# Performance work log

Hardware: AMD Instinct MI355X
Metric: run time of the kernel (lower is better)

The kernel has to match this reference:

```python
import jax, jax.numpy as jnp
import numpy as np

N_HEADS = 4
HEAD_DIM = 6
D_MODEL = 24


def setup_inputs() -> dict:
    key = jax.random.key(0)
    ks = jax.random.split(key, 7)
    B, Tq, Tk = 16, 1024, 1024
    X = jax.random.normal(ks[0], (B, Tq, D_MODEL), dtype=jnp.float32)
    X_en = jax.random.normal(ks[1], (B, Tk, D_MODEL), dtype=jnp.float32)
    I_m = jax.random.randint(ks[2], (B, Tq, Tk), 0, 2, dtype=jnp.int32)
    scale = 1.0 / np.sqrt(D_MODEL)
    Wq = jax.random.normal(ks[3], (D_MODEL, D_MODEL), dtype=jnp.float32) * scale
    Wk = jax.random.normal(ks[4], (D_MODEL, D_MODEL), dtype=jnp.float32) * scale
    Wv = jax.random.normal(ks[5], (D_MODEL, D_MODEL), dtype=jnp.float32) * scale
    Wo = jax.random.normal(ks[6], (D_MODEL, D_MODEL), dtype=jnp.float32) * scale
    return {"X": X, "X_en": X_en, "I_m": I_m, "Wq": Wq, "Wk": Wk, "Wv": Wv, "Wo": Wo}


def _split_heads(x):
    # [B, T, 24] -> [B, 4, T, 6]
    B, T, _ = x.shape
    return x.reshape(B, T, N_HEADS, HEAD_DIM).transpose(0, 2, 1, 3)


def reference(X, X_en, I_m, Wq, Wk, Wv, Wo):
    # torch Linear (no bias): x @ W.T
    Q = _split_heads(X @ Wq.T)      # [B, H, Tq, d]
    K = _split_heads(X_en @ Wk.T)   # [B, H, Tk, d]
    V = _split_heads(X_en @ Wv.T)   # [B, H, Tk, d]
    scale = 1.0 / jnp.sqrt(jnp.asarray(HEAD_DIM, dtype=Q.dtype))
    A = jnp.einsum('bhqd,bhkd->bhqk', Q, K) * scale
    # NOTE: the original torch code calls A.masked_fill(...) without assigning
    # the result, so the mask I_m has NO effect. Faithfully reproduced here.
    A = jax.nn.softmax(A, axis=-1)
    O = jnp.einsum('bhqk,bhkd->bhqd', A, V)  # [B, H, Tq, d]
    B, H, Tq, d = O.shape
    O = O.transpose(0, 2, 1, 3).reshape(B, Tq, H * d)  # [B, Tq, 24]
    return O @ Wo.T
```

## Files before the change

### kernel.cpp

```cpp
#include <hip/hip_runtime.h>
#include <hip/hip_bf16.h>

#define NB 16
#define TT 1024
#define NH 4
#define HD 6
#define DM 24

#define QSC 0.5889785f
#define MBIAS 32.0f

typedef float v2f __attribute__((ext_vector_type(2)));
typedef short bf16x8 __attribute__((ext_vector_type(8)));
typedef float f32x16 __attribute__((ext_vector_type(16)));
typedef unsigned u32x2 __attribute__((ext_vector_type(2)));

__device__ __forceinline__ unsigned cvt_pk_bf16(float lo, float hi) {
  unsigned r;
  asm("v_cvt_pk_bf16_f32 %0, %1, %2" : "=v"(r) : "v"(lo), "v"(hi));
  return r;
}

__device__ __forceinline__ bf16x8 as_bf16x8(uint4 u) {
  union { uint4 u; bf16x8 b; } c;
  c.u = u;
  return c.b;
}

__device__ __forceinline__ unsigned short bf16of(float v) {
  union { __hip_bfloat16 b; unsigned short u; } c;
  c.b = __float2bfloat16(v);
  return c.u;
}

__device__ __forceinline__ float dot24(const float4* r,
                                       const float* __restrict__ w) {
  v2f a = {0.f, 0.f};
#pragma unroll
  for (int i = 0; i < 6; ++i) {
    v2f xp, wp;
    xp.x = r[i].x; xp.y = r[i].y;
    wp.x = w[4 * i + 0]; wp.y = w[4 * i + 1];
    a = __builtin_elementwise_fma(xp, wp, a);
    xp.x = r[i].z; xp.y = r[i].w;
    wp.x = w[4 * i + 2]; wp.y = w[4 * i + 3];
    a = __builtin_elementwise_fma(xp, wp, a);
  }
  return a.x + a.y;
}

__global__ __launch_bounds__(256, 4) void kvproj_kernel(
    const float* __restrict__ Xen, const float* __restrict__ Wk,
    const float* __restrict__ Wv, uint4* __restrict__ Kg,
    unsigned short* __restrict__ Vt) {
  const int gid = blockIdx.x * 256 + threadIdx.x;
  const int bh = gid >> 10;
  const int key = gid & (TT - 1);
  const int b = bh >> 2, h = bh & 3;
  const float* __restrict__ wkh = Wk + h * HD * DM;
  const float* __restrict__ wvh = Wv + h * HD * DM;
  const float4* __restrict__ xa =
      (const float4*)(Xen + ((size_t)b * TT + key) * DM);
  float4 xr[6];
#pragma unroll
  for (int i = 0; i < 6; ++i) xr[i] = xa[i];
  float kk[HD], vv[HD];
#pragma unroll
  for (int d = 0; d < HD; ++d) {
    kk[d] = dot24(xr, wkh + d * DM);
    vv[d] = dot24(xr, wvh + d * DM);
  }
  uint4* __restrict__ kdst = Kg + ((size_t)bh * TT + key) * 2;
  kdst[0] = make_uint4(cvt_pk_bf16(kk[0], kk[1]), cvt_pk_bf16(kk[2], kk[3]),
                       cvt_pk_bf16(kk[4], kk[5]), 0u);
  kdst[1] = make_uint4(0u, 0u, 0u, 0u);
  unsigned short* __restrict__ vrow = Vt + (size_t)bh * (7 * TT);
#pragma unroll
  for (int d = 0; d < HD; ++d) vrow[d * TT + key] = bf16of(vv[d]);
  vrow[6 * TT + key] = 0x3F80u;
}

__global__ __launch_bounds__(256, 4) void attn_mfma32_kernel(
    const float* __restrict__ X, const float* __restrict__ Wq,
    const uint4* __restrict__ Kg, const unsigned short* __restrict__ Vt,
    float* __restrict__ P) {
  const int ks = blockIdx.x & 1;
  const int tile = (blockIdx.x >> 1) & 7;
  const int bh = blockIdx.x >> 4;
  const int b = bh >> 2, h = bh & 3;
  const int lane = threadIdx.x & 63;
  const int w = threadIdx.x >> 6;
  const int hi = lane >> 5;
  const int qc = lane & 31;
  const int q = tile * 128 + w * 32 + qc;

  const float* __restrict__ wqh = Wq + h * HD * DM;
  uint4 uq = make_uint4(0u, 0u, 0u, 0u);
  if (hi == 0) {
    const float4* __restrict__ xq =
        (const float4*)(X + ((size_t)b * TT + q) * DM);
    float4 xr[6];
#pragma unroll
    for (int i = 0; i < 6; ++i) xr[i] = xq[i];
    float qv[HD];
#pragma unroll
    for (int d = 0; d < HD; ++d) qv[d] = dot24(xr, wqh + d * DM) * QSC;
    uq = make_uint4(cvt_pk_bf16(qv[0], qv[1]), cvt_pk_bf16(qv[2], qv[3]),
                    cvt_pk_bf16(qv[4], qv[5]), 0u);
  }
  const bf16x8 qfrag = as_bf16x8(uq);

  f32x16 cmb, oacc;
#pragma unroll
  for (int i = 0; i < 16; ++i) { cmb[i] = -MBIAS; oacc[i] = 0.f; }

  const uint4* __restrict__ kp =
      Kg + (size_t)bh * (TT * 2) + (size_t)ks * TT + qc * 2 + hi;
  const int dcl = (qc < 7) ? qc : 6;
  const uint4* __restrict__ vp =
      (const uint4*)(Vt + (size_t)bh * (7 * TT) + dcl * TT) + ks * 64 + hi;

#pragma unroll 2
  for (int it = 0; it < 16; ++it) {
    const uint4 ka = kp[it * 64];
    const uint4 va = vp[it * 4];
    const uint4 vb = vp[it * 4 + 2];

    f32x16 s = __builtin_amdgcn_mfma_f32_32x32x16_bf16(as_bf16x8(ka), qfrag,
                                                       cmb, 0, 0, 0);
    float p[16];
#pragma unroll
    for (int i = 0; i < 16; ++i) p[i] = __builtin_amdgcn_exp2f(s[i]);
    const unsigned c01 = cvt_pk_bf16(p[0], p[1]);
    const unsigned c23 = cvt_pk_bf16(p[2], p[3]);
    const unsigned c45 = cvt_pk_bf16(p[4], p[5]);
    const unsigned c67 = cvt_pk_bf16(p[6], p[7]);
    const unsigned c89 = cvt_pk_bf16(p[8], p[9]);
    const unsigned cAB = cvt_pk_bf16(p[10], p[11]);
    const unsigned cCD = cvt_pk_bf16(p[12], p[13]);
    const unsigned cEF = cvt_pk_bf16(p[14], p[15]);
    const u32x2 r0 = __builtin_amdgcn_permlane32_swap(c01, c45, false, false);
    const u32x2 r1 = __builtin_amdgcn_permlane32_swap(c23, c67, false, false);
    const u32x2 r2 = __builtin_amdgcn_permlane32_swap(c89, cCD, false, false);
    const u32x2 r3 = __builtin_amdgcn_permlane32_swap(cAB, cEF, false, false);
    const uint4 pb0 = make_uint4(r0[0], r1[0], r0[1], r1[1]);
    const uint4 pb1 = make_uint4(r2[0], r3[0], r2[1], r3[1]);
    oacc = __builtin_amdgcn_mfma_f32_32x32x16_bf16(as_bf16x8(va),
                                                   as_bf16x8(pb0), oacc, 0, 0, 0);
    oacc = __builtin_amdgcn_mfma_f32_32x32x16_bf16(as_bf16x8(vb),
                                                   as_bf16x8(pb1), oacc, 0, 0, 0);
  }

  const float a4 = __shfl_xor(oacc[0], 32);
  const float a5 = __shfl_xor(oacc[1], 32);
  const float ll = __shfl_xor(oacc[2], 32);
  if (hi == 0) {
    float* __restrict__ Pr =
        P + (((size_t)(bh * 2 + ks)) * TT + q) * 8;
    ((float4*)Pr)[0] = make_float4(ll, oacc[0], oacc[1], oacc[2]);
    ((float4*)Pr)[1] = make_float4(oacc[3], a4, a5, 0.f);
  }
}

__global__ __launch_bounds__(256, 4) void combine_outproj_kernel(
    const float* __restrict__ P, const float* __restrict__ Wo,
    float* __restrict__ out) {
  __shared__ float wsh[DM * DM];
  __shared__ float o[32][25];
  for (int i = threadIdx.x; i < DM * DM; i += 256) wsh[i] = Wo[i];
  const int r0 = blockIdx.x * 32;
  {
    const int unit = threadIdx.x >> 1, e = threadIdx.x & 1;
    const int rl = unit >> 2, h = unit & 3;
    const int r = r0 + rl, b = r >> 10, t = r & (TT - 1);
    const int bh = b * NH + h;
    const float4* __restrict__ pp =
        (const float4*)(P + (((size_t)(bh * 2 + e)) * TT + t) * 8);
    float4 x0 = pp[0], x1 = pp[1];
    float l = x0.x, a0 = x0.y, a1 = x0.z, a2 = x0.w;
    float a3 = x1.x, a4 = x1.y, a5 = x1.z;
    l += __shfl_xor(l, 1);
    a0 += __shfl_xor(a0, 1);
    a1 += __shfl_xor(a1, 1);
    a2 += __shfl_xor(a2, 1);
    a3 += __shfl_xor(a3, 1);
    a4 += __shfl_xor(a4, 1);
    a5 += __shfl_xor(a5, 1);
    if (e == 0) {
      const float inv = 1.f / l;
      o[rl][h * HD + 0] = a0 * inv;
      o[rl][h * HD + 1] = a1 * inv;
      o[rl][h * HD + 2] = a2 * inv;
      o[rl][h * HD + 3] = a3 * inv;
      o[rl][h * HD + 4] = a4 * inv;
      o[rl][h * HD + 5] = a5 * inv;
    }
  }
  __syncthreads();
  const int rl = threadIdx.x >> 3, u = threadIdx.x & 7;
  const int r = r0 + rl;
  float x[DM];
#pragma unroll
  for (int c = 0; c < DM; ++c) x[c] = o[rl][c];
#pragma unroll
  for (int jj = 0; jj < 3; ++jj) {
    const int j = u * 3 + jj;
    float a = 0.f;
#pragma unroll
    for (int c = 0; c < DM; ++c) a = fmaf(x[c], wsh[j * DM + c], a);
    out[(size_t)r * DM + j] = a;
  }
}

extern "C" void kernel_launch(void* const* d_in, const int* in_sizes, int n_in,
                              void* d_out, int out_size, void* d_ws, size_t ws_size,
                              hipStream_t stream) {
  const float* X = (const float*)d_in[0];
  const float* Xen = (const float*)d_in[1];
  const float* Wq = (const float*)d_in[3];
  const float* Wk = (const float*)d_in[4];
  const float* Wv = (const float*)d_in[5];
  const float* Wo = (const float*)d_in[6];

  char* ws = (char*)d_ws;
  float* P = (float*)ws;
  uint4* Kg = (uint4*)(ws + 4u * 1024 * 1024);
  unsigned short* Vt =
      (unsigned short*)(ws + 6u * 1024 * 1024);

  kvproj_kernel<<<NB * NH * TT / 256, 256, 0, stream>>>(Xen, Wk, Wv, Kg, Vt);
  attn_mfma32_kernel<<<NB * NH * 8 * 2, 256, 0, stream>>>(X, Wq, Kg, Vt, P);
  combine_outproj_kernel<<<NB * TT / 32, 256, 0, stream>>>(P, Wo,
                                                           (float*)d_out);
}
```

Measured before the change: 28.85 us.

## Switch attention to 16x16x32 MFMA tiles with compact K layout

Replaces the 32x32x16 bf16 MFMA attention kernel with one built on 16x16x32 MFMAs. Each wave now handles 16 queries, the grid doubles, and the launch bound rises to 8 blocks per SM. The K buffer drops its zero-padded second uint4 per key, which halves K traffic, and P fragments are rearranged with permlane32/permlane16 swaps. Partial-output layout and workspace offsets change to match. This cuts wasted MFMA work on the padded 32-wide dimension and raises occupancy, but the Q projection is now computed redundantly by more lanes.

```diff
diff --git a/kernel.cpp b/kernel.cpp
--- a/kernel.cpp
+++ b/kernel.cpp
@@ -12,7 +12,7 @@
 
 typedef float v2f __attribute__((ext_vector_type(2)));
 typedef short bf16x8 __attribute__((ext_vector_type(8)));
-typedef float f32x16 __attribute__((ext_vector_type(16)));
+typedef float f32x4 __attribute__((ext_vector_type(4)));
 typedef unsigned u32x2 __attribute__((ext_vector_type(2)));
 
 __device__ __forceinline__ unsigned cvt_pk_bf16(float lo, float hi) {
@@ -70,33 +70,36 @@
     kk[d] = dot24(xr, wkh + d * DM);
     vv[d] = dot24(xr, wvh + d * DM);
   }
-  uint4* __restrict__ kdst = Kg + ((size_t)bh * TT + key) * 2;
-  kdst[0] = make_uint4(cvt_pk_bf16(kk[0], kk[1]), cvt_pk_bf16(kk[2], kk[3]),
-                       cvt_pk_bf16(kk[4], kk[5]), 0u);
-  kdst[1] = make_uint4(0u, 0u, 0u, 0u);
+  Kg[(size_t)bh * TT + key] =
+      make_uint4(cvt_pk_bf16(kk[0], kk[1]), cvt_pk_bf16(kk[2], kk[3]),
+                 cvt_pk_bf16(kk[4], kk[5]), 0u);
   unsigned short* __restrict__ vrow = Vt + (size_t)bh * (7 * TT);
 #pragma unroll
   for (int d = 0; d < HD; ++d) vrow[d * TT + key] = bf16of(vv[d]);
   vrow[6 * TT + key] = 0x3F80u;
 }
 
-__global__ __launch_bounds__(256, 4) void attn_mfma32_kernel(
+#define KSPLIT 2
+#define KPB (TT / KSPLIT)
+#define ITERS (KPB / 32)
+
+__global__ __launch_bounds__(256, 8) void attn16_kernel(
     const float* __restrict__ X, const float* __restrict__ Wq,
     const uint4* __restrict__ Kg, const unsigned short* __restrict__ Vt,
     float* __restrict__ P) {
   const int ks = blockIdx.x & 1;
-  const int tile = (blockIdx.x >> 1) & 7;
-  const int bh = blockIdx.x >> 4;
+  const int tile = (blockIdx.x >> 1) & 15;
+  const int bh = blockIdx.x >> 5;
   const int b = bh >> 2, h = bh & 3;
   const int lane = threadIdx.x & 63;
   const int w = threadIdx.x >> 6;
-  const int hi = lane >> 5;
-  const int qc = lane & 31;
-  const int q = tile * 128 + w * 32 + qc;
+  const int lg = lane >> 4;
+  const int lq = lane & 15;
+  const int q = tile * 64 + w * 16 + lq;
 
   const float* __restrict__ wqh = Wq + h * HD * DM;
   uint4 uq = make_uint4(0u, 0u, 0u, 0u);
-  if (hi == 0) {
+  {
     const float4* __restrict__ xq =
         (const float4*)(X + ((size_t)b * TT + q) * DM);
     float4 xr[6];
@@ -105,61 +108,72 @@
     float qv[HD];
 #pragma unroll
     for (int d = 0; d < HD; ++d) qv[d] = dot24(xr, wqh + d * DM) * QSC;
-    uq = make_uint4(cvt_pk_bf16(qv[0], qv[1]), cvt_pk_bf16(qv[2], qv[3]),
-                    cvt_pk_bf16(qv[4], qv[5]), 0u);
+    if (lg == 0)
+      uq = make_uint4(cvt_pk_bf16(qv[0], qv[1]), cvt_pk_bf16(qv[2], qv[3]),
+                      cvt_pk_bf16(qv[4], qv[5]), 0u);
   }
   const bf16x8 qfrag = as_bf16x8(uq);
 
-  f32x16 cmb, oacc;
-#pragma unroll
-  for (int i = 0; i < 16; ++i) { cmb[i] = -MBIAS; oacc[i] = 0.f; }
-
-  const uint4* __restrict__ kp =
-      Kg + (size_t)bh * (TT * 2) + (size_t)ks * TT + qc * 2 + hi;
-  const int dcl = (qc < 7) ? qc : 6;
+  f32x4 cmb, oacc;
+  cmb[0] = -MBIAS; cmb[1] = -MBIAS; cmb[2] = -MBIAS; cmb[3] = -MBIAS;
+  oacc[0] = 0.f; oacc[1] = 0.f; oacc[2] = 0.f; oacc[3] = 0.f;
+
+  const uint4* __restrict__ kp = Kg + (size_t)bh * TT + ks * KPB + lq;
+  const int dcl = (lq < 7) ? lq : 6;
   const uint4* __restrict__ vp =
-      (const uint4*)(Vt + (size_t)bh * (7 * TT) + dcl * TT) + ks * 64 + hi;
+      (const uint4*)(Vt + (size_t)bh * (7 * TT) + dcl * TT) + ks * (KPB / 8) +
+      lg;
 
 #pragma unroll 2
-  for (int it = 0; it < 16; ++it) {
-    const uint4 ka = kp[it * 64];
-    const uint4 va = vp[it * 4];
-    const uint4 vb = vp[it * 4 + 2];
-
-    f32x16 s = __builtin_amdgcn_mfma_f32_32x32x16_bf16(as_bf16x8(ka), qfrag,
+  for (int it = 0; it < ITERS; ++it) {
+    const uint4 ka = kp[it * 32];
+    const uint4 kb = kp[it * 32 + 16];
+    const uint4 vv = vp[it * 4];
+
+    f32x4 s0 = __builtin_amdgcn_mfma_f32_16x16x32_bf16(as_bf16x8(ka), qfrag,
                                                        cmb, 0, 0, 0);
-    float p[16];
-#pragma unroll
-    for (int i = 0; i < 16; ++i) p[i] = __builtin_amdgcn_exp2f(s[i]);
-    const unsigned c01 = cvt_pk_bf16(p[0], p[1]);
-    const unsigned c23 = cvt_pk_bf16(p[2], p[3]);
-    const unsigned c45 = cvt_pk_bf16(p[4], p[5]);
-    const unsigned c67 = cvt_pk_bf16(p[6], p[7]);
-    const unsigned c89 = cvt_pk_bf16(p[8], p[9]);
-    const unsigned cAB = cvt_pk_bf16(p[10], p[11]);
-    const unsigned cCD = cvt_pk_bf16(p[12], p[13]);
-    const unsigned cEF = cvt_pk_bf16(p[14], p[15]);
-    const u32x2 r0 = __builtin_amdgcn_permlane32_swap(c01, c45, false, false);
-    const u32x2 r1 = __builtin_amdgcn_permlane32_swap(c23, c67, false, false);
-    const u32x2 r2 = __builtin_amdgcn_permlane32_swap(c89, cCD, false, false);
-    const u32x2 r3 = __builtin_amdgcn_permlane32_swap(cAB, cEF, false, false);
-    const uint4 pb0 = make_uint4(r0[0], r1[0], r0[1], r1[1]);
-    const uint4 pb1 = make_uint4(r2[0], r3[0], r2[1], r3[1]);
-    oacc = __builtin_amdgcn_mfma_f32_32x32x16_bf16(as_bf16x8(va),
-                                                   as_bf16x8(pb0), oacc, 0, 0, 0);
-    oacc = __builtin_amdgcn_mfma_f32_32x32x16_bf16(as_bf16x8(vb),
-                                                   as_bf16x8(pb1), oacc, 0, 0, 0);
-  }
-
-  const float a4 = __shfl_xor(oacc[0], 32);
-  const float a5 = __shfl_xor(oacc[1], 32);
-  const float ll = __shfl_xor(oacc[2], 32);
-  if (hi == 0) {
-    float* __restrict__ Pr =
-        P + (((size_t)(bh * 2 + ks)) * TT + q) * 8;
-    ((float4*)Pr)[0] = make_float4(ll, oacc[0], oacc[1], oacc[2]);
-    ((float4*)Pr)[1] = make_float4(oacc[3], a4, a5, 0.f);
-  }
+    f32x4 s1 = __builtin_amdgcn_mfma_f32_16x16x32_bf16(as_bf16x8(kb), qfrag,
+                                                       cmb, 0, 0, 0);
+    const float p0 = __builtin_amdgcn_exp2f(s0[0]);
+    const float p1 = __builtin_amdgcn_exp2f(s0[1]);
+    const float p2 = __builtin_amdgcn_exp2f(s0[2]);
+    const float p3 = __builtin_amdgcn_exp2f(s0[3]);
+    const float p4 = __builtin_amdgcn_exp2f(s1[0]);
+    const float p5 = __builtin_amdgcn_exp2f(s1[1]);
+    const float p6 = __builtin_amdgcn_exp2f(s1[2]);
+    const float p7 = __builtin_amdgcn_exp2f(s1[3]);
+    const unsigned c00 = cvt_pk_bf16(p0, p1);
+    const unsigned c01 = cvt_pk_bf16(p2, p3);
+    const unsigned c10 = cvt_pk_bf16(p4, p5);
+    const unsigned c11 = cvt_pk_bf16(p6, p7);
+
+    const u32x2 A = __builtin_amdgcn_permlane32_swap(c00, c10, false, false);
+    const u32x2 B = __builtin_amdgcn_permlane32_swap(c01, c11, false, false);
+#if __has_builtin(__builtin_amdgcn_permlane16_swap)
+    const u32x2 W02 =
+        __builtin_amdgcn_permlane16_swap(A[0], A[1], false, false);
+    const u32x2 W13 =
+        __builtin_amdgcn_permlane16_swap(B[0], B[1], false, false);
+    const uint4 pb = make_uint4(W02[0], W13[0], W02[1], W13[1]);
+#else
+    const unsigned a1x = (unsigned)__shfl_xor((int)A[1], 16);
+    const unsigned a0x = (unsigned)__shfl_xor((int)A[0], 16);
+    const unsigned b1x = (unsigned)__shfl_xor((int)B[1], 16);
+    const unsigned b0x = (unsigned)__shfl_xor((int)B[0], 16);
+    const bool odd = (lg & 1);
+    const uint4 pb = make_uint4(odd ? a1x : A[0], odd ? b1x : B[0],
+                                odd ? A[1] : a0x, odd ? B[1] : b0x);
+#endif
+    oacc = __builtin_amdgcn_mfma_f32_16x16x32_bf16(as_bf16x8(vv),
+                                                   as_bf16x8(pb), oacc, 0, 0, 0);
+  }
+
+  float* __restrict__ Pr =
+      P + (((size_t)(bh * KSPLIT + ks)) * TT + q) * 8;
+  if (lg == 0)
+    ((float4*)Pr)[0] = make_float4(oacc[0], oacc[1], oacc[2], oacc[3]);
+  if (lg == 1)
+    ((float4*)Pr)[1] = make_float4(oacc[0], oacc[1], oacc[2], oacc[3]);
 }
 
 __global__ __launch_bounds__(256, 4) void combine_outproj_kernel(
@@ -175,10 +189,10 @@
     const int r = r0 + rl, b = r >> 10, t = r & (TT - 1);
     const int bh = b * NH + h;
     const float4* __restrict__ pp =
-        (const float4*)(P + (((size_t)(bh * 2 + e)) * TT + t) * 8);
+        (const float4*)(P + (((size_t)(bh * KSPLIT + e)) * TT + t) * 8);
     float4 x0 = pp[0], x1 = pp[1];
-    float l = x0.x, a0 = x0.y, a1 = x0.z, a2 = x0.w;
-    float a3 = x1.x, a4 = x1.y, a5 = x1.z;
+    float a0 = x0.x, a1 = x0.y, a2 = x0.z, a3 = x0.w;
+    float a4 = x1.x, a5 = x1.y, l = x1.z;
     l += __shfl_xor(l, 1);
     a0 += __shfl_xor(a0, 1);
     a1 += __shfl_xor(a1, 1);
@@ -224,12 +238,12 @@
 
   char* ws = (char*)d_ws;
   float* P = (float*)ws;
-  uint4* Kg = (uint4*)(ws + 4u * 1024 * 1024);
+  uint4* Kg = (uint4*)(ws + 8u * 1024 * 1024);
   unsigned short* Vt =
-      (unsigned short*)(ws + 6u * 1024 * 1024);
+      (unsigned short*)(ws + 10u * 1024 * 1024);
 
   kvproj_kernel<<<NB * NH * TT / 256, 256, 0, stream>>>(Xen, Wk, Wv, Kg, Vt);
-  attn_mfma32_kernel<<<NB * NH * 8 * 2, 256, 0, stream>>>(X, Wq, Kg, Vt, P);
+  attn16_kernel<<<NB * NH * 16 * KSPLIT, 256, 0, stream>>>(X, Wq, Kg, Vt, P);
   combine_outproj_kernel<<<NB * TT / 32, 256, 0, stream>>>(P, Wo,
                                                            (float*)d_out);
 }
```

New measurement: 33.05 us. 1.15x slower.

## Fuse K/V projection into attention kernel via shared-memory staging

Applied to the files above, without the earlier changes.

Removes the separate K/V projection kernel. Each attention block now computes its own 512-key slice of K and V from X_en into LDS, then runs the MFMA attention loop reading from shared memory instead of global K/V buffers. This drops one kernel launch and the global round trip for K/V. In exchange, K/V projection is recomputed redundantly by every query tile (8x per head), and a block-level sync is added before the main loop.

```diff
diff --git a/kernel.cpp b/kernel.cpp
--- a/kernel.cpp
+++ b/kernel.cpp
@@ -25,12 +25,6 @@
   union { uint4 u; bf16x8 b; } c;
   c.u = u;
   return c.b;
-}
-
-__device__ __forceinline__ unsigned short bf16of(float v) {
-  union { __hip_bfloat16 b; unsigned short u; } c;
-  c.b = __float2bfloat16(v);
-  return c.u;
 }
 
 __device__ __forceinline__ float dot24(const float4* r,
@@ -49,52 +43,59 @@
   return a.x + a.y;
 }
 
-__global__ __launch_bounds__(256, 4) void kvproj_kernel(
-    const float* __restrict__ Xen, const float* __restrict__ Wk,
-    const float* __restrict__ Wv, uint4* __restrict__ Kg,
-    unsigned short* __restrict__ Vt) {
-  const int gid = blockIdx.x * 256 + threadIdx.x;
-  const int bh = gid >> 10;
-  const int key = gid & (TT - 1);
-  const int b = bh >> 2, h = bh & 3;
-  const float* __restrict__ wkh = Wk + h * HD * DM;
-  const float* __restrict__ wvh = Wv + h * HD * DM;
-  const float4* __restrict__ xa =
-      (const float4*)(Xen + ((size_t)b * TT + key) * DM);
-  float4 xr[6];
-#pragma unroll
-  for (int i = 0; i < 6; ++i) xr[i] = xa[i];
-  float kk[HD], vv[HD];
-#pragma unroll
-  for (int d = 0; d < HD; ++d) {
-    kk[d] = dot24(xr, wkh + d * DM);
-    vv[d] = dot24(xr, wvh + d * DM);
-  }
-  uint4* __restrict__ kdst = Kg + ((size_t)bh * TT + key) * 2;
-  kdst[0] = make_uint4(cvt_pk_bf16(kk[0], kk[1]), cvt_pk_bf16(kk[2], kk[3]),
-                       cvt_pk_bf16(kk[4], kk[5]), 0u);
-  kdst[1] = make_uint4(0u, 0u, 0u, 0u);
-  unsigned short* __restrict__ vrow = Vt + (size_t)bh * (7 * TT);
-#pragma unroll
-  for (int d = 0; d < HD; ++d) vrow[d * TT + key] = bf16of(vv[d]);
-  vrow[6 * TT + key] = 0x3F80u;
-}
-
-__global__ __launch_bounds__(256, 4) void attn_mfma32_kernel(
-    const float* __restrict__ X, const float* __restrict__ Wq,
-    const uint4* __restrict__ Kg, const unsigned short* __restrict__ Vt,
-    float* __restrict__ P) {
+#define KSPLIT 2
+#define KPB (TT / KSPLIT)
+#define QB 128
+#define ITERS (KPB / 32)
+
+__global__ __launch_bounds__(256, 4) void fused_attn32_kernel(
+    const float* __restrict__ X, const float* __restrict__ Xen,
+    const float* __restrict__ Wq, const float* __restrict__ Wk,
+    const float* __restrict__ Wv, float* __restrict__ P) {
+  __shared__ __align__(16) uint4 Kl[KPB];
+  __shared__ __align__(16) unsigned Vl[7][264];
+
   const int ks = blockIdx.x & 1;
   const int tile = (blockIdx.x >> 1) & 7;
   const int bh = blockIdx.x >> 4;
   const int b = bh >> 2, h = bh & 3;
-  const int lane = threadIdx.x & 63;
-  const int w = threadIdx.x >> 6;
+  const int t = threadIdx.x;
+
+  const float* __restrict__ wqh = Wq + h * HD * DM;
+  const float* __restrict__ wkh = Wk + h * HD * DM;
+  const float* __restrict__ wvh = Wv + h * HD * DM;
+
+  {
+    const float4* __restrict__ xe =
+        (const float4*)(Xen + ((size_t)b * TT + ks * KPB + 2 * t) * DM);
+    float4 xr[12];
+#pragma unroll
+    for (int i = 0; i < 12; ++i) xr[i] = xe[i];
+    float kA[HD], kB[HD];
+#pragma unroll
+    for (int d = 0; d < HD; ++d) {
+      kA[d] = dot24(xr + 0, wkh + d * DM);
+      kB[d] = dot24(xr + 6, wkh + d * DM);
+    }
+    Kl[2 * t] = make_uint4(cvt_pk_bf16(kA[0], kA[1]), cvt_pk_bf16(kA[2], kA[3]),
+                           cvt_pk_bf16(kA[4], kA[5]), 0u);
+    Kl[2 * t + 1] =
+        make_uint4(cvt_pk_bf16(kB[0], kB[1]), cvt_pk_bf16(kB[2], kB[3]),
+                   cvt_pk_bf16(kB[4], kB[5]), 0u);
+#pragma unroll
+    for (int d = 0; d < HD; ++d) {
+      const float vA = dot24(xr + 0, wvh + d * DM);
+      const float vB = dot24(xr + 6, wvh + d * DM);
+      Vl[d][t] = cvt_pk_bf16(vA, vB);
+    }
+    Vl[6][t] = 0x3F803F80u;
+  }
+
+  const int lane = t & 63;
+  const int w = t >> 6;
   const int hi = lane >> 5;
   const int qc = lane & 31;
-  const int q = tile * 128 + w * 32 + qc;
-
-  const float* __restrict__ wqh = Wq + h * HD * DM;
+  const int q = tile * QB + w * 32 + qc;
   uint4 uq = make_uint4(0u, 0u, 0u, 0u);
   if (hi == 0) {
     const float4* __restrict__ xq =
@@ -110,21 +111,19 @@
   }
   const bf16x8 qfrag = as_bf16x8(uq);
 
+  __syncthreads();
+
   f32x16 cmb, oacc;
 #pragma unroll
   for (int i = 0; i < 16; ++i) { cmb[i] = -MBIAS; oacc[i] = 0.f; }
 
-  const uint4* __restrict__ kp =
-      Kg + (size_t)bh * (TT * 2) + (size_t)ks * TT + qc * 2 + hi;
   const int dcl = (qc < 7) ? qc : 6;
-  const uint4* __restrict__ vp =
-      (const uint4*)(Vt + (size_t)bh * (7 * TT) + dcl * TT) + ks * 64 + hi;
+  const uint4 zero4 = make_uint4(0u, 0u, 0u, 0u);
 
 #pragma unroll 2
-  for (int it = 0; it < 16; ++it) {
-    const uint4 ka = kp[it * 64];
-    const uint4 va = vp[it * 4];
-    const uint4 vb = vp[it * 4 + 2];
+  for (int it = 0; it < ITERS; ++it) {
+    const uint4 ka = (hi == 0) ? Kl[it * 32 + qc] : zero4;
+    const uint4 vv = *(const uint4*)&Vl[dcl][it * 16 + 4 * hi];
 
     f32x16 s = __builtin_amdgcn_mfma_f32_32x32x16_bf16(as_bf16x8(ka), qfrag,
                                                        cmb, 0, 0, 0);
@@ -145,9 +144,10 @@
     const u32x2 r3 = __builtin_amdgcn_permlane32_swap(cAB, cEF, false, false);
     const uint4 pb0 = make_uint4(r0[0], r1[0], r0[1], r1[1]);
     const uint4 pb1 = make_uint4(r2[0], r3[0], r2[1], r3[1]);
-    oacc = __builtin_amdgcn_mfma_f32_32x32x16_bf16(as_bf16x8(va),
+    oacc = __builtin_amdgcn_mfma_f32_32x32x16_bf16(as_bf16x8(vv),
                                                    as_bf16x8(pb0), oacc, 0, 0, 0);
-    oacc = __builtin_amdgcn_mfma_f32_32x32x16_bf16(as_bf16x8(vb),
+    const uint4 vv2 = *(const uint4*)&Vl[dcl][it * 16 + 8 + 4 * hi];
+    oacc = __builtin_amdgcn_mfma_f32_32x32x16_bf16(as_bf16x8(vv2),
                                                    as_bf16x8(pb1), oacc, 0, 0, 0);
   }
 
@@ -155,8 +155,7 @@
   const float a5 = __shfl_xor(oacc[1], 32);
   const float ll = __shfl_xor(oacc[2], 32);
   if (hi == 0) {
-    float* __restrict__ Pr =
-        P + (((size_t)(bh * 2 + ks)) * TT + q) * 8;
+    float* __restrict__ Pr = P + (((size_t)(bh * KSPLIT + ks)) * TT + q) * 8;
     ((float4*)Pr)[0] = make_float4(ll, oacc[0], oacc[1], oacc[2]);
     ((float4*)Pr)[1] = make_float4(oacc[3], a4, a5, 0.f);
   }
@@ -175,7 +174,7 @@
     const int r = r0 + rl, b = r >> 10, t = r & (TT - 1);
     const int bh = b * NH + h;
     const float4* __restrict__ pp =
-        (const float4*)(P + (((size_t)(bh * 2 + e)) * TT + t) * 8);
+        (const float4*)(P + (((size_t)(bh * KSPLIT + e)) * TT + t) * 8);
     float4 x0 = pp[0], x1 = pp[1];
     float l = x0.x, a0 = x0.y, a1 = x0.z, a2 = x0.w;
     float a3 = x1.x, a4 = x1.y, a5 = x1.z;
@@ -222,14 +221,10 @@
   const float* Wv = (const float*)d_in[5];
   const float* Wo = (const float*)d_in[6];
 
-  char* ws = (char*)d_ws;
-  float* P = (float*)ws;
-  uint4* Kg = (uint4*)(ws + 4u * 1024 * 1024);
-  unsigned short* Vt =
-      (unsigned short*)(ws + 6u * 1024 * 1024);
-
-  kvproj_kernel<<<NB * NH * TT / 256, 256, 0, stream>>>(Xen, Wk, Wv, Kg, Vt);
-  attn_mfma32_kernel<<<NB * NH * 8 * 2, 256, 0, stream>>>(X, Wq, Kg, Vt, P);
+  float* P = (float*)d_ws;
+
+  fused_attn32_kernel<<<NB * NH * 8 * KSPLIT, 256, 0, stream>>>(X, Xen, Wq,
+                                                                Wk, Wv, P);
   combine_outproj_kernel<<<NB * TT / 32, 256, 0, stream>>>(P, Wo,
                                                            (float*)d_out);
 }
```

Measured after the change: 25.00 us, median of 2. 13.3% less time.
